# Kernel tuning notes

Hardware: AMD Instinct MI355X
Metric: run time of the kernel (lower is better)

The kernel has to match this reference:

```python
import jax, jax.numpy as jnp
import numpy as np

N_NODES = 100000
N_EDGES = 1600000
NUM_PROP = 5
CAT_PROP = 3
INPUT_DIM = 128
HIDDEN = 128
NUM_REL = 2


def setup_inputs() -> dict:
    key = jax.random.key(0)
    ks = jax.random.split(key, 20)
    s = 0.05
    inp = {
        "x": jax.random.normal(ks[0], (N_NODES, NUM_PROP + CAT_PROP), jnp.float32),
        "edge_index": jax.random.randint(ks[1], (2, N_EDGES), 0, N_NODES, jnp.int64 if jax.config.jax_enable_x64 else jnp.int32),
        "edge_type": jax.random.randint(ks[2], (N_EDGES,), 0, NUM_REL, jnp.int32),
        # numeric / categorical encoders -> input_dim/2 each
        "W_num": jax.random.normal(ks[3], (NUM_PROP, INPUT_DIM // 2), jnp.float32) * s,
        "b_num": jnp.zeros((INPUT_DIM // 2,), jnp.float32),
        "W_cat": jax.random.normal(ks[4], (CAT_PROP, INPUT_DIM // 2), jnp.float32) * s,
        "b_cat": jnp.zeros((INPUT_DIM // 2,), jnp.float32),
        # input projection + PReLU
        "W_in": jax.random.normal(ks[5], (INPUT_DIM, HIDDEN), jnp.float32) * s,
        "b_in": jnp.zeros((HIDDEN,), jnp.float32),
        "prelu_a": jnp.full((HIDDEN,), 0.25, jnp.float32),
        # RGCN layer 1
        "W_rel1": jax.random.normal(ks[6], (NUM_REL, HIDDEN, HIDDEN), jnp.float32) * s,
        "W_root1": jax.random.normal(ks[7], (HIDDEN, HIDDEN), jnp.float32) * s,
        "b_rgcn1": jnp.zeros((HIDDEN,), jnp.float32),
        # RGCN layer 2
        "W_rel2": jax.random.normal(ks[8], (NUM_REL, HIDDEN, HIDDEN), jnp.float32) * s,
        "W_root2": jax.random.normal(ks[9], (HIDDEN, HIDDEN), jnp.float32) * s,
        "b_rgcn2": jnp.zeros((HIDDEN,), jnp.float32),
        # classifier (single Linear)
        "W_cls": jax.random.normal(ks[10], (HIDDEN, HIDDEN), jnp.float32) * s,
        "b_cls": jnp.zeros((HIDDEN,), jnp.float32),
    }
    return inp


def _leaky_relu(x, slope=0.01):
    return jnp.where(x >= 0, x, slope * x)


def _prelu(x, a):
    return jnp.where(x >= 0, x, a * x)


def _rgcn_conv(x, edge_index, edge_type, W_rel, W_root, bias):
    # PyG RGCNConv: out[i] = x[i] @ W_root + bias + sum_r mean_{j in N_r(i)} x[j] @ W_r
    # Aggregate-then-transform (linearity) to avoid per-edge (E, d) @ W products.
    src, dst = edge_index[0], edge_index[1]
    n = x.shape[0]
    x_src = x[src]  # (E, d) gather
    out = x @ W_root + bias
    for r in range(W_rel.shape[0]):
        w = (edge_type == r).astype(x.dtype)  # (E,)
        agg = jax.ops.segment_sum(x_src * w[:, None], dst, num_segments=n)  # (N, d)
        deg = jax.ops.segment_sum(w, dst, num_segments=n)  # (N,)
        out = out + (agg / jnp.clip(deg, 1.0)[:, None]) @ W_rel[r]
    return out


def reference(x, edge_index, edge_type, W_num, b_num, W_cat, b_cat, W_in, b_in,
              prelu_a, W_rel1, W_root1, b_rgcn1, W_rel2, W_root2, b_rgcn2,
              W_cls, b_cls):
    num_prop = x[:, :NUM_PROP]
    cat_prop = x[:, NUM_PROP:NUM_PROP + CAT_PROP]
    n = _leaky_relu(num_prop @ W_num + b_num)
    c = _leaky_relu(cat_prop @ W_cat + b_cat)
    h = jnp.concatenate([n, c], axis=1)
    h = _prelu(h @ W_in + b_in, prelu_a)
    h = _rgcn_conv(h, edge_index, edge_type, W_rel1, W_root1, b_rgcn1)
    # dropout is identity in eval mode
    h = _rgcn_conv(h, edge_index, edge_type, W_rel2, W_root2, b_rgcn2)
    return h @ W_cls + b_cls
```

## Files before the change

### kernel.cpp

```cpp
#include <hip/hip_runtime.h>
#include <cstdint>


typedef short bf16x8 __attribute__((ext_vector_type(8)));
typedef float f32x4  __attribute__((ext_vector_type(4)));

__device__ __forceinline__ unsigned short f2bf(float f) {
    unsigned int u = __builtin_bit_cast(unsigned int, f);
    u += 0x7fff + ((u >> 16) & 1);
    return (unsigned short)(u >> 16);
}
__device__ __forceinline__ float bf2f(unsigned short h) {
    unsigned int u = ((unsigned int)h) << 16;
    return __builtin_bit_cast(float, u);
}
__device__ __forceinline__ float lo16f(unsigned int u) {
    return __builtin_bit_cast(float, u << 16);
}
__device__ __forceinline__ float hi16f(unsigned int u) {
    return __builtin_bit_cast(float, u & 0xffff0000u);
}

__device__ __forceinline__ void gload_lds16(const void* g, void* l) {
    __builtin_amdgcn_global_load_lds(
        (const __attribute__((address_space(1))) void*)g,
        (__attribute__((address_space(3))) void*)l, 16, 0, 0);
}

__global__ __launch_bounds__(256) void k_egemm(
    const float* __restrict__ x,
    const float* __restrict__ Wnum, const float* __restrict__ bnum,
    const float* __restrict__ Wcat, const float* __restrict__ bcat,
    const unsigned short* __restrict__ Bhi, const unsigned short* __restrict__ Blo,
    const float* __restrict__ bias, const float* __restrict__ prelu,
    unsigned short* __restrict__ C_hi, unsigned short* __restrict__ C_lo, int M)
{
    __shared__ unsigned short lds[2][32 * 512];
    const int t = threadIdx.x;
    const int w = t >> 6, lane = t & 63;
    const int laneL = lane & 15, laneH = lane >> 4;
    const int wi = w >> 1, wj = w & 1;
    const int m0 = blockIdx.x * 128;
    const int Mm1 = M - 1;

    f32x4 acc[4][4];
    #pragma unroll
    for (int a = 0; a < 4; ++a)
        #pragma unroll
        for (int b = 0; b < 4; ++b)
            acc[a][b] = (f32x4){0.f, 0.f, 0.f, 0.f};

    auto stage = [&](int s, unsigned short* buf) {
        int koff = s * 32;
        int k8 = koff + laneH * 8;
        #pragma unroll
        for (int c = 0; c < 2; ++c) {
            int j = w + c * 4;
            int rc = j * 16 + laneL;
            int row = (m0 + rc <= Mm1) ? (m0 + rc) : Mm1;
            const float4* xr = (const float4*)(x + (size_t)row * 8);
            float4 X0 = xr[0], X1 = xr[1];
            float a[8];
            if (k8 < 64) {
                const float4* bp = (const float4*)(bnum + k8);
                float4 b0 = bp[0], b1 = bp[1];
                a[0]=b0.x; a[1]=b0.y; a[2]=b0.z; a[3]=b0.w;
                a[4]=b1.x; a[5]=b1.y; a[6]=b1.z; a[7]=b1.w;
                float xs0 = X0.x, xs1 = X0.y, xs2 = X0.z, xs3 = X0.w, xs4 = X1.x;
                const float* wb = Wnum + k8;
                #pragma unroll
                for (int p = 0; p < 5; ++p) {
                    float xp = p==0?xs0 : p==1?xs1 : p==2?xs2 : p==3?xs3 : xs4;
                    const float4* wp = (const float4*)(wb + p * 64);
                    float4 w0 = wp[0], w1 = wp[1];
                    a[0]+=xp*w0.x; a[1]+=xp*w0.y; a[2]+=xp*w0.z; a[3]+=xp*w0.w;
                    a[4]+=xp*w1.x; a[5]+=xp*w1.y; a[6]+=xp*w1.z; a[7]+=xp*w1.w;
                }
            } else {
                int kk = k8 - 64;
                const float4* bp = (const float4*)(bcat + kk);
                float4 b0 = bp[0], b1 = bp[1];
                a[0]=b0.x; a[1]=b0.y; a[2]=b0.z; a[3]=b0.w;
                a[4]=b1.x; a[5]=b1.y; a[6]=b1.z; a[7]=b1.w;
                float xs0 = X1.y, xs1 = X1.z, xs2 = X1.w;
                const float* wb = Wcat + kk;
                #pragma unroll
                for (int p = 0; p < 3; ++p) {
                    float xp = p==0?xs0 : p==1?xs1 : xs2;
                    const float4* wp = (const float4*)(wb + p * 64);
                    float4 w0 = wp[0], w1 = wp[1];
                    a[0]+=xp*w0.x; a[1]+=xp*w0.y; a[2]+=xp*w0.z; a[3]+=xp*w0.w;
                    a[4]+=xp*w1.x; a[5]+=xp*w1.y; a[6]+=xp*w1.z; a[7]+=xp*w1.w;
                }
            }
            unsigned hw[4], lw[4];
            #pragma unroll
            for (int q = 0; q < 4; ++q) {
                float v0 = a[2*q]   >= 0.f ? a[2*q]   : 0.01f * a[2*q];
                float v1 = a[2*q+1] >= 0.f ? a[2*q+1] : 0.01f * a[2*q+1];
                unsigned short h0 = f2bf(v0), h1 = f2bf(v1);
                unsigned short l0 = f2bf(v0 - bf2f(h0)), l1 = f2bf(v1 - bf2f(h1));
                hw[q] = (unsigned)h0 | ((unsigned)h1 << 16);
                lw[q] = (unsigned)l0 | ((unsigned)l1 << 16);
            }
            uint4 ho, lo_;
            ho.x=hw[0]; ho.y=hw[1]; ho.z=hw[2]; ho.w=hw[3];
            lo_.x=lw[0]; lo_.y=lw[1]; lo_.z=lw[2]; lo_.w=lw[3];
            *(uint4*)&buf[(0 * 8 + j) * 512 + lane * 8] = ho;
            *(uint4*)&buf[(1 * 8 + j) * 512 + lane * 8] = lo_;
        }
        #pragma unroll
        for (int c = 4; c < 8; ++c) {
            int chunk = w + c * 4;
            int slot = chunk >> 3, j = chunk & 7;
            const unsigned short* plane = (slot == 2) ? Bhi : Blo;
            int rc = j * 16 + laneL;
            const unsigned short* gp = plane + (size_t)rc * 128 + koff + laneH * 8;
            gload_lds16(gp, &buf[(slot * 8 + j) * 512]);
        }
    };

    stage(0, lds[0]);
    for (int s = 0; s < 4; ++s) {
        unsigned short* cur = lds[s & 1];
        unsigned short* nxt = lds[(s & 1) ^ 1];
        __syncthreads();
        if (s + 1 < 4) stage(s + 1, nxt);
        const bf16x8* fr = (const bf16x8*)cur;
        bf16x8 ah[4], al[4], bh[4], bl[4];
        #pragma unroll
        for (int mi = 0; mi < 4; ++mi) {
            ah[mi] = fr[(0 + wi * 4 + mi) * 64 + lane];
            al[mi] = fr[(8 + wi * 4 + mi) * 64 + lane];
        }
        #pragma unroll
        for (int nj = 0; nj < 4; ++nj) {
            bh[nj] = fr[(16 + wj * 4 + nj) * 64 + lane];
            bl[nj] = fr[(24 + wj * 4 + nj) * 64 + lane];
        }
        #pragma unroll
        for (int mi = 0; mi < 4; ++mi)
            #pragma unroll
            for (int nj = 0; nj < 4; ++nj) {
                acc[mi][nj] = __builtin_amdgcn_mfma_f32_16x16x32_bf16(
                    ah[mi], bh[nj], acc[mi][nj], 0, 0, 0);
                acc[mi][nj] = __builtin_amdgcn_mfma_f32_16x16x32_bf16(
                    ah[mi], bl[nj], acc[mi][nj], 0, 0, 0);
                acc[mi][nj] = __builtin_amdgcn_mfma_f32_16x16x32_bf16(
                    al[mi], bh[nj], acc[mi][nj], 0, 0, 0);
            }
    }

    float bv[4], av[4];
    #pragma unroll
    for (int nj = 0; nj < 4; ++nj) {
        int col = wj * 64 + nj * 16 + laneL;
        bv[nj] = bias[col];
        av[nj] = prelu[col];
    }
    unsigned short* lph = &lds[0][0];
    unsigned short* lpl = &lds[1][0];
    __syncthreads();
    #pragma unroll
    for (int nj = 0; nj < 4; ++nj) {
        int col = wj * 64 + nj * 16 + laneL;
        #pragma unroll
        for (int mi = 0; mi < 4; ++mi)
            #pragma unroll
            for (int r = 0; r < 4; ++r) {
                int row = wi * 64 + mi * 16 + laneH * 4 + r;
                float v = acc[mi][nj][r] + bv[nj];
                v = v >= 0.f ? v : av[nj] * v;
                unsigned short h = f2bf(v);
                lph[row * 128 + col] = h;
                lpl[row * 128 + col] = f2bf(v - bf2f(h));
            }
    }
    __syncthreads();
    {
        const uint4* sh = (const uint4*)lph;
        const uint4* sl = (const uint4*)lpl;
        #pragma unroll
        for (int it = 0; it < 8; ++it) {
            int idx = it * 256 + t;
            int row = idx >> 4, c = idx & 15;
            int m = m0 + row;
            if (m < M) {
                ((uint4*)(C_hi + (size_t)m * 128))[c] = sh[idx];
                ((uint4*)(C_lo + (size_t)m * 128))[c] = sl[idx];
            }
        }
    }
}

struct WHArgs {
    const float* W[8];
    unsigned short* hi[8];
    unsigned short* lo[8];
    const int* ei;
    const int* et;
    int* cntmatT;
    int E;
    int N;
    int NBINS;
};
__global__ __launch_bounds__(256) void k_wsplit_hist(WHArgs a)
{
    __shared__ int hist[1024];
    const int t = threadIdx.x;
    const int b = blockIdx.x;
    if (b < 512) {
        int part = b >> 6;
        int idx = (b & 63) * 256 + t;
        int n = idx >> 7, k = idx & 127;
        float v = a.W[part][(size_t)k * 128 + n];
        unsigned short h = f2bf(v);
        a.hi[part][(size_t)n * 128 + k] = h;
        a.lo[part][(size_t)n * 128 + k] = f2bf(v - bf2f(h));
        return;
    }
    const int blk = b - 512;
    for (int i = t; i < a.NBINS; i += 256) hist[i] = 0;
    __syncthreads();
    #pragma unroll
    for (int j = 0; j < 16; ++j) {
        int e = blk * 4096 + j * 256 + t;
        if (e < a.E) atomicAdd(&hist[(a.et[e] * a.N + a.ei[a.E + e]) >> 8], 1);
    }
    __syncthreads();
    for (int i = t; i < a.NBINS; i += 256)
        a.cntmatT[(size_t)blk * a.NBINS + i] = hist[i];
}

__global__ __launch_bounds__(256) void k_transpose(
    const int* __restrict__ src, int* __restrict__ dst, int R, int C)
{
    __shared__ int tile[32][33];
    int ctiles = (C + 31) >> 5;
    int bx = blockIdx.x % ctiles;
    int by = blockIdx.x / ctiles;
    int tc = threadIdx.x & 31, tr = threadIdx.x >> 5;
    int c0 = bx * 32, r0 = by * 32;
    #pragma unroll
    for (int i = 0; i < 32; i += 8) {
        int r = r0 + tr + i, c = c0 + tc;
        if (r < R && c < C) tile[tr + i][tc] = src[(size_t)r * C + c];
    }
    __syncthreads();
    #pragma unroll
    for (int i = 0; i < 32; i += 8) {
        int r = r0 + tc;
        int c = c0 + tr + i;
        if (r < R && c < C) dst[(size_t)c * R + r] = tile[tc][tr + i];
    }
}

__global__ __launch_bounds__(256) void k_transpose_add(
    const int* __restrict__ src, int* __restrict__ dst,
    const int* __restrict__ bsum, int R, int C)
{
    __shared__ int tile[32][33];
    int ctiles = (C + 31) >> 5;
    int bx = blockIdx.x % ctiles;
    int by = blockIdx.x / ctiles;
    int tc = threadIdx.x & 31, tr = threadIdx.x >> 5;
    int c0 = bx * 32, r0 = by * 32;
    #pragma unroll
    for (int i = 0; i < 32; i += 8) {
        int r = r0 + tr + i, c = c0 + tc;
        if (r < R && c < C) {
            size_t idx = (size_t)r * C + c;
            tile[tr + i][tc] = src[idx] + bsum[idx >> 8];
        }
    }
    __syncthreads();
    #pragma unroll
    for (int i = 0; i < 32; i += 8) {
        int r = r0 + tc;
        int c = c0 + tr + i;
        if (r < R && c < C) dst[(size_t)c * R + r] = tile[tc][tr + i];
    }
}

__global__ __launch_bounds__(256) void k_scan1(
    const int* __restrict__ src, int* __restrict__ dst,
    int* __restrict__ bsum, int n)
{
    __shared__ int s[256];
    int t = threadIdx.x;
    int i = blockIdx.x * 256 + t;
    int v = (i < n) ? src[i] : 0;
    s[t] = v;
    __syncthreads();
    #pragma unroll
    for (int d = 1; d < 256; d <<= 1) {
        int add = (t >= d) ? s[t - d] : 0;
        __syncthreads();
        s[t] += add;
        __syncthreads();
    }
    if (i < n) dst[i] = s[t] - v;
    if (t == 255) bsum[blockIdx.x] = s[255];
}

__global__ __launch_bounds__(1024) void k_scan2(int* __restrict__ bsum, int nb)
{
    __shared__ int s[1024];
    int t = threadIdx.x;
    int carry = 0;
    for (int base = 0; base < nb; base += 1024) {
        int i = base + t;
        int v = (i < nb) ? bsum[i] : 0;
        s[t] = v;
        __syncthreads();
        #pragma unroll
        for (int d = 1; d < 1024; d <<= 1) {
            int add = (t >= d) ? s[t - d] : 0;
            __syncthreads();
            s[t] += add;
            __syncthreads();
        }
        if (i < nb) bsum[i] = carry + s[t] - v;
        carry += s[1023];
        __syncthreads();
    }
}

__global__ __launch_bounds__(256) void k_binscatter(
    const int* __restrict__ ei, const int* __restrict__ et,
    const int* __restrict__ cntscanT, int* __restrict__ ebuf,
    int E, int N, int NBINS)
{
    __shared__ int base[1024];
    const int t = threadIdx.x;
    const int blk = blockIdx.x;
    for (int i = t; i < NBINS; i += 256)
        base[i] = cntscanT[(size_t)blk * NBINS + i];
    __syncthreads();
    #pragma unroll
    for (int j = 0; j < 16; ++j) {
        int e = blk * 4096 + j * 256 + t;
        if (e < E) {
            unsigned src = (unsigned)ei[e];
            int seg = et[e] * N + ei[E + e];
            int pos = atomicAdd(&base[seg >> 8], 1);
            ebuf[pos] = (int)(((unsigned)(seg & 255) << 24) | src);
        }
    }
}

__global__ __launch_bounds__(256) void k_bincsr(
    const int* __restrict__ cntscan, const int* __restrict__ bsum,
    const int* __restrict__ ebuf,
    int* __restrict__ deg, int* __restrict__ off, int* __restrict__ esrc,
    int E, int nseg, int NBLK, int NBINS)
{
    __shared__ int cnt[256];
    __shared__ int pfx[256];
    __shared__ int cur[256];
    const int b = blockIdx.x;
    const int t = threadIdx.x;
    size_t i0 = (size_t)b * NBLK;
    const int est = cntscan[i0] + bsum[i0 >> 8];
    int een = E;
    if (b + 1 < NBINS) {
        size_t i1 = (size_t)(b + 1) * NBLK;
        een = cntscan[i1] + bsum[i1 >> 8];
    }
    cnt[t] = 0;
    __syncthreads();
    for (int e = est + t; e < een; e += 256)
        atomicAdd(&cnt[((unsigned)ebuf[e]) >> 24], 1);
    __syncthreads();
    int v = cnt[t];
    pfx[t] = v;
    __syncthreads();
    #pragma unroll
    for (int d = 1; d < 256; d <<= 1) {
        int add = (t >= d) ? pfx[t - d] : 0;
        __syncthreads();
        pfx[t] += add;
        __syncthreads();
    }
    int o = est + pfx[t] - v;
    int seg = b * 256 + t;
    if (seg < nseg) { deg[seg] = v; off[seg] = o; }
    cur[t] = o;
    __syncthreads();
    for (int e = est + t; e < een; e += 256) {
        unsigned u = (unsigned)ebuf[e];
        int p = atomicAdd(&cur[u >> 24], 1);
        esrc[p] = (int)(u & 0xffffffu);
    }
}

__global__ __launch_bounds__(256) void k_gather(
    const unsigned short* __restrict__ h_hi,
    const int* __restrict__ esrc,
    const int* __restrict__ off, const int* __restrict__ deg,
    unsigned short* __restrict__ a_hi, int nseg)
{
    int i = blockIdx.x * 8 + (threadIdx.x >> 5);
    if (i >= nseg) return;
    int l32 = threadIdx.x & 31;
    int q = l32 >> 4;
    int l16 = l32 & 15;
    int cnt = deg[i], st = off[i];
    const uint4* hp = (const uint4*)h_hi;
    float a0 = 0.f, a1 = 0.f, a2 = 0.f, a3 = 0.f;
    float a4 = 0.f, a5 = 0.f, a6 = 0.f, a7 = 0.f;
    int e = q;
    for (; e + 6 < cnt; e += 8) {
        int i0 = esrc[st + e + 0];
        int i1 = esrc[st + e + 2];
        int i2 = esrc[st + e + 4];
        int i3 = esrc[st + e + 6];
        uint4 u0 = hp[(size_t)i0 * 16 + l16];
        uint4 u1 = hp[(size_t)i1 * 16 + l16];
        uint4 u2 = hp[(size_t)i2 * 16 + l16];
        uint4 u3 = hp[(size_t)i3 * 16 + l16];
        a0 += lo16f(u0.x); a1 += hi16f(u0.x); a2 += lo16f(u0.y); a3 += hi16f(u0.y);
        a4 += lo16f(u0.z); a5 += hi16f(u0.z); a6 += lo16f(u0.w); a7 += hi16f(u0.w);
        a0 += lo16f(u1.x); a1 += hi16f(u1.x); a2 += lo16f(u1.y); a3 += hi16f(u1.y);
        a4 += lo16f(u1.z); a5 += hi16f(u1.z); a6 += lo16f(u1.w); a7 += hi16f(u1.w);
        a0 += lo16f(u2.x); a1 += hi16f(u2.x); a2 += lo16f(u2.y); a3 += hi16f(u2.y);
        a4 += lo16f(u2.z); a5 += hi16f(u2.z); a6 += lo16f(u2.w); a7 += hi16f(u2.w);
        a0 += lo16f(u3.x); a1 += hi16f(u3.x); a2 += lo16f(u3.y); a3 += hi16f(u3.y);
        a4 += lo16f(u3.z); a5 += hi16f(u3.z); a6 += lo16f(u3.w); a7 += hi16f(u3.w);
    }
    for (; e < cnt; e += 2) {
        uint4 u = hp[(size_t)esrc[st + e] * 16 + l16];
        a0 += lo16f(u.x); a1 += hi16f(u.x); a2 += lo16f(u.y); a3 += hi16f(u.y);
        a4 += lo16f(u.z); a5 += hi16f(u.z); a6 += lo16f(u.w); a7 += hi16f(u.w);
    }
    a0 += __shfl_xor(a0, 16, 64);
    a1 += __shfl_xor(a1, 16, 64);
    a2 += __shfl_xor(a2, 16, 64);
    a3 += __shfl_xor(a3, 16, 64);
    a4 += __shfl_xor(a4, 16, 64);
    a5 += __shfl_xor(a5, 16, 64);
    a6 += __shfl_xor(a6, 16, 64);
    a7 += __shfl_xor(a7, 16, 64);
    if (q == 0) {
        float inv = 1.0f / (float)(cnt > 1 ? cnt : 1);
        uint4 o;
        o.x = (unsigned int)f2bf(a0 * inv) | ((unsigned int)f2bf(a1 * inv) << 16);
        o.y = (unsigned int)f2bf(a2 * inv) | ((unsigned int)f2bf(a3 * inv) << 16);
        o.z = (unsigned int)f2bf(a4 * inv) | ((unsigned int)f2bf(a5 * inv) << 16);
        o.w = (unsigned int)f2bf(a6 * inv) | ((unsigned int)f2bf(a7 * inv) << 16);
        ((uint4*)a_hi)[(size_t)i * 16 + l16] = o;
    }
}

struct GArgs {
    const unsigned short* A_hi[3];
    const unsigned short* A_lo[3];
    const unsigned short* B_hi[3];
    const unsigned short* B_lo[3];
    int alo[3];
    int blo[3];
    const float* bias;
    const float* prelu;
    unsigned short* C_hi;
    unsigned short* C_lo;
    int M;
    int P;
    const unsigned short* clsBhi;
    const unsigned short* clsBlo;
    const float* clsBias;
    float* outF;
};

__global__ __launch_bounds__(256) void k_mgemm(GArgs g)
{
    __shared__ unsigned short lds[2][32 * 512];
    const int t = threadIdx.x;
    const int w = t >> 6, lane = t & 63;
    const int laneL = lane & 15, laneH = lane >> 4;
    const int wi = w >> 1, wj = w & 1;
    const int m0 = blockIdx.x * 128;
    const int Mm1 = g.M - 1;
    const int S = g.P * 4;

    f32x4 acc[4][4];
    #pragma unroll
    for (int a = 0; a < 4; ++a)
        #pragma unroll
        for (int b = 0; b < 4; ++b)
            acc[a][b] = (f32x4){0.f, 0.f, 0.f, 0.f};

    auto stage = [&](int s, unsigned short* buf) {
        int p = s >> 2, koff = (s & 3) * 32;
        const unsigned short* tp[4];
        tp[0] = g.A_hi[p];
        tp[1] = g.alo[p] ? g.A_lo[p] : nullptr;
        tp[2] = g.B_hi[p];
        tp[3] = g.blo[p] ? g.B_lo[p] : nullptr;
        #pragma unroll
        for (int c = 0; c < 8; ++c) {
            int chunk = w + c * 4;
            int slot = chunk >> 3, j = chunk & 7;
            const unsigned short* plane = tp[slot];
            if (!plane) continue;
            int rc = j * 16 + laneL;
            int row = (slot < 2) ? (m0 + rc <= Mm1 ? m0 + rc : Mm1) : rc;
            const unsigned short* gp = plane + (size_t)row * 128 + koff + laneH * 8;
            gload_lds16(gp, &buf[(slot * 8 + j) * 512]);
        }
    };

    stage(0, lds[0]);
    for (int s = 0; s < S; ++s) {
        unsigned short* cur = lds[s & 1];
        unsigned short* nxt = lds[(s & 1) ^ 1];
        __syncthreads();
        if (s + 1 < S) stage(s + 1, nxt);
        int p = s >> 2;
        const bool hasAlo = g.alo[p] != 0;
        const bool hasBlo = g.blo[p] != 0;
        const bf16x8* fr = (const bf16x8*)cur;
        bf16x8 ah[4], al[4], bh[4], bl[4];
        #pragma unroll
        for (int mi = 0; mi < 4; ++mi)
            ah[mi] = fr[(0 + wi * 4 + mi) * 64 + lane];
        if (hasAlo) {
            #pragma unroll
            for (int mi = 0; mi < 4; ++mi)
                al[mi] = fr[(8 + wi * 4 + mi) * 64 + lane];
        }
        #pragma unroll
        for (int nj = 0; nj < 4; ++nj)
            bh[nj] = fr[(16 + wj * 4 + nj) * 64 + lane];
        if (hasBlo) {
            #pragma unroll
            for (int nj = 0; nj < 4; ++nj)
                bl[nj] = fr[(24 + wj * 4 + nj) * 64 + lane];
        }
        #pragma unroll
        for (int mi = 0; mi < 4; ++mi)
            #pragma unroll
            for (int nj = 0; nj < 4; ++nj) {
                acc[mi][nj] = __builtin_amdgcn_mfma_f32_16x16x32_bf16(
                    ah[mi], bh[nj], acc[mi][nj], 0, 0, 0);
                if (hasBlo)
                    acc[mi][nj] = __builtin_amdgcn_mfma_f32_16x16x32_bf16(
                        ah[mi], bl[nj], acc[mi][nj], 0, 0, 0);
                if (hasAlo)
                    acc[mi][nj] = __builtin_amdgcn_mfma_f32_16x16x32_bf16(
                        al[mi], bh[nj], acc[mi][nj], 0, 0, 0);
            }
    }

    float bv[4];
    #pragma unroll
    for (int nj = 0; nj < 4; ++nj)
        bv[nj] = g.bias[wj * 64 + nj * 16 + laneL];

    if (g.clsBhi) {
        char* l0 = (char*)&lds[0][0];
        char* l1 = (char*)&lds[1][0];
        __syncthreads();
        #pragma unroll
        for (int nj = 0; nj < 4; ++nj) {
            int col = wj * 64 + nj * 16 + laneL;
            #pragma unroll
            for (int mi = 0; mi < 4; ++mi)
                #pragma unroll
                for (int r = 0; r < 4; ++r) {
                    int row = wi * 64 + mi * 16 + laneH * 4 + r;
                    float v = acc[mi][nj][r] + bv[nj];
                    unsigned short h = f2bf(v);
                    int offb = row * 256 + ((col * 2) ^ ((row & 7) << 4));
                    *(unsigned short*)(l0 + offb) = h;
                    *(unsigned short*)(l1 + offb) = f2bf(v - bf2f(h));
                }
        }
        __syncthreads();
        f32x4 acc2[4][4];
        #pragma unroll
        for (int a = 0; a < 4; ++a)
            #pragma unroll
            for (int b = 0; b < 4; ++b)
                acc2[a][b] = (f32x4){0.f, 0.f, 0.f, 0.f};
        #pragma unroll
        for (int ks = 0; ks < 4; ++ks) {
            bf16x8 ah2[4], al2[4], bh2[4], bl2[4];
            #pragma unroll
            for (int mi = 0; mi < 4; ++mi) {
                int rc = wi * 64 + mi * 16 + laneL;
                int aoff = rc * 256 + ((ks * 64 + laneH * 16) ^ ((rc & 7) << 4));
                ah2[mi] = *(const bf16x8*)(l0 + aoff);
                al2[mi] = *(const bf16x8*)(l1 + aoff);
            }
            #pragma unroll
            for (int nj = 0; nj < 4; ++nj) {
                int rc = wj * 64 + nj * 16 + laneL;
                size_t boff = (size_t)rc * 128 + ks * 32 + laneH * 8;
                bh2[nj] = *(const bf16x8*)(g.clsBhi + boff);
                bl2[nj] = *(const bf16x8*)(g.clsBlo + boff);
            }
            #pragma unroll
            for (int mi = 0; mi < 4; ++mi)
                #pragma unroll
                for (int nj = 0; nj < 4; ++nj) {
                    acc2[mi][nj] = __builtin_amdgcn_mfma_f32_16x16x32_bf16(
                        ah2[mi], bh2[nj], acc2[mi][nj], 0, 0, 0);
                    acc2[mi][nj] = __builtin_amdgcn_mfma_f32_16x16x32_bf16(
                        ah2[mi], bl2[nj], acc2[mi][nj], 0, 0, 0);
                    acc2[mi][nj] = __builtin_amdgcn_mfma_f32_16x16x32_bf16(
                        al2[mi], bh2[nj], acc2[mi][nj], 0, 0, 0);
                }
        }
        float cb[4];
        #pragma unroll
        for (int nj = 0; nj < 4; ++nj)
            cb[nj] = g.clsBias[wj * 64 + nj * 16 + laneL];
        float* lf = (float*)&lds[0][0];
        __syncthreads();
        #pragma unroll
        for (int nj = 0; nj < 4; ++nj) {
            int col = wj * 64 + nj * 16 + laneL;
            #pragma unroll
            for (int mi = 0; mi < 4; ++mi)
                #pragma unroll
                for (int r = 0; r < 4; ++r) {
                    int row = wi * 64 + mi * 16 + laneH * 4 + r;
                    lf[row * 128 + col] = acc2[mi][nj][r] + cb[nj];
                }
        }
        __syncthreads();
        const uint4* lsrc = (const uint4*)lf;
        #pragma unroll
        for (int it = 0; it < 16; ++it) {
            int idx = it * 256 + t;
            int row = idx >> 5, c = idx & 31;
            int m = m0 + row;
            if (m < g.M)
                ((uint4*)(g.outF + (size_t)m * 128))[c] = lsrc[idx];
        }
        return;
    }

    const bool hasPrelu = (g.prelu != nullptr);
    float av[4];
    #pragma unroll
    for (int nj = 0; nj < 4; ++nj)
        av[nj] = hasPrelu ? g.prelu[wj * 64 + nj * 16 + laneL] : 0.f;

    unsigned short* lph = &lds[0][0];
    unsigned short* lpl = &lds[1][0];
    __syncthreads();
    #pragma unroll
    for (int nj = 0; nj < 4; ++nj) {
        int col = wj * 64 + nj * 16 + laneL;
        #pragma unroll
        for (int mi = 0; mi < 4; ++mi)
            #pragma unroll
            for (int r = 0; r < 4; ++r) {
                int row = wi * 64 + mi * 16 + laneH * 4 + r;
                float v = acc[mi][nj][r] + bv[nj];
                if (hasPrelu) v = v >= 0.f ? v : av[nj] * v;
                unsigned short h = f2bf(v);
                lph[row * 128 + col] = h;
                lpl[row * 128 + col] = f2bf(v - bf2f(h));
            }
    }
    __syncthreads();
    {
        const uint4* sh = (const uint4*)lph;
        const uint4* sl = (const uint4*)lpl;
        #pragma unroll
        for (int it = 0; it < 8; ++it) {
            int idx = it * 256 + t;
            int row = idx >> 4, c = idx & 15;
            int m = m0 + row;
            if (m < g.M) {
                ((uint4*)(g.C_hi + (size_t)m * 128))[c] = sh[idx];
                ((uint4*)(g.C_lo + (size_t)m * 128))[c] = sl[idx];
            }
        }
    }
}

extern "C" void kernel_launch(void* const* d_in, const int* in_sizes, int n_in,
                              void* d_out, int out_size, void* d_ws, size_t ws_size,
                              hipStream_t stream) {
    const float* x      = (const float*)d_in[0];
    const int*   ei     = (const int*)d_in[1];
    const int*   et     = (const int*)d_in[2];
    const float* Wnum   = (const float*)d_in[3];
    const float* bnum   = (const float*)d_in[4];
    const float* Wcat   = (const float*)d_in[5];
    const float* bcat   = (const float*)d_in[6];
    const float* Win    = (const float*)d_in[7];
    const float* bin    = (const float*)d_in[8];
    const float* pa     = (const float*)d_in[9];
    const float* Wrel1  = (const float*)d_in[10];
    const float* Wroot1 = (const float*)d_in[11];
    const float* brg1   = (const float*)d_in[12];
    const float* Wrel2  = (const float*)d_in[13];
    const float* Wroot2 = (const float*)d_in[14];
    const float* brg2   = (const float*)d_in[15];
    const float* Wcls   = (const float*)d_in[16];
    const float* bcls   = (const float*)d_in[17];
    float* out = (float*)d_out;

    const int N = in_sizes[0] / 8;
    const int E = in_sizes[1] / 2;
    const int nseg = 2 * N;
    const size_t NH = (size_t)N * 128;

    const int NBLK  = (E + 4095) / 4096;
    const int NBINS = (nseg + 255) / 256;
    const long long L = (long long)NBINS * NBLK;

    char* w = (char*)d_ws;
    unsigned short* h1_hi = (unsigned short*)w;  w += NH * 2;
    unsigned short* h1_lo = (unsigned short*)w;  w += NH * 2;
    unsigned short* agg_hi = (unsigned short*)w; w += 2 * NH * 2;
    int* deg      = (int*)w;  w += (size_t)nseg * 4;
    int* off      = (int*)w;  w += (size_t)nseg * 4;
    int* cntmatT  = (int*)w;  w += (size_t)L * 4;
    int* cntmat   = (int*)w;  w += (size_t)L * 4;
    int* cntscan  = (int*)w;  w += (size_t)L * 4;
    int* cntscanT = (int*)w;  w += (size_t)L * 4;
    int* esrc     = (int*)w;  w += (size_t)E * 4;
    int* bsum     = (int*)w;  w += 4096 * 4;
    unsigned short* wplanes = (unsigned short*)w;  w += 8 * 2 * 16384 * 2;

    int* ebuf = (int*)d_out;
    unsigned short* h0_hi = (unsigned short*)d_out;
    unsigned short* h0_lo = h0_hi + NH;

    unsigned short* whi[8];
    unsigned short* wlo[8];
    for (int i = 0; i < 8; ++i) {
        whi[i] = wplanes + (size_t)i * 2 * 16384;
        wlo[i] = whi[i] + 16384;
    }

    const int gm = (N + 127) / 128;
    const int gg = (nseg + 7) / 8;

    {
        WHArgs a;
        a.W[0] = Win;   a.W[1] = Wroot1; a.W[2] = Wrel1; a.W[3] = Wrel1 + 16384;
        a.W[4] = Wroot2; a.W[5] = Wrel2; a.W[6] = Wrel2 + 16384; a.W[7] = Wcls;
        for (int i = 0; i < 8; ++i) { a.hi[i] = whi[i]; a.lo[i] = wlo[i]; }
        a.ei = ei; a.et = et; a.cntmatT = cntmatT;
        a.E = E; a.N = N; a.NBINS = NBINS;
        k_wsplit_hist<<<512 + NBLK, 256, 0, stream>>>(a);
    }

    k_transpose<<<((NBLK + 31) / 32) * ((NBINS + 31) / 32), 256, 0, stream>>>(
        cntmatT, cntmat, NBLK, NBINS);

    const int nb1 = (int)((L + 255) / 256);
    k_scan1<<<nb1, 256, 0, stream>>>(cntmat, cntscan, bsum, (int)L);
    k_scan2<<<1, 1024, 0, stream>>>(bsum, nb1);
    k_transpose_add<<<((NBINS + 31) / 32) * ((NBLK + 31) / 32), 256, 0, stream>>>(
        cntscan, cntscanT, bsum, NBINS, NBLK);

    k_binscatter<<<NBLK, 256, 0, stream>>>(ei, et, cntscanT, ebuf, E, N, NBINS);
    k_bincsr<<<NBINS, 256, 0, stream>>>(cntscan, bsum, ebuf, deg, off, esrc,
                                        E, nseg, NBLK, NBINS);

    k_egemm<<<gm, 256, 0, stream>>>(x, Wnum, bnum, Wcat, bcat,
                                    whi[0], wlo[0], bin, pa,
                                    h0_hi, h0_lo, N);

    k_gather<<<gg, 256, 0, stream>>>(h0_hi, esrc, off, deg, agg_hi, nseg);
    {
        GArgs g = {};
        g.A_hi[0] = h0_hi;       g.A_lo[0] = h0_lo;  g.alo[0] = 1; g.blo[0] = 1;
        g.A_hi[1] = agg_hi;      g.alo[1] = 0;       g.blo[1] = 0;
        g.A_hi[2] = agg_hi + NH; g.alo[2] = 0;       g.blo[2] = 0;
        g.B_hi[0] = whi[1]; g.B_lo[0] = wlo[1];
        g.B_hi[1] = whi[2]; g.B_lo[1] = wlo[2];
        g.B_hi[2] = whi[3]; g.B_lo[2] = wlo[3];
        g.bias = brg1; g.prelu = nullptr;
        g.C_hi = h1_hi; g.C_lo = h1_lo;
        g.M = N; g.P = 3;
        g.clsBhi = nullptr;
        k_mgemm<<<gm, 256, 0, stream>>>(g);
    }
    k_gather<<<gg, 256, 0, stream>>>(h1_hi, esrc, off, deg, agg_hi, nseg);
    {
        GArgs g = {};
        g.A_hi[0] = h1_hi;       g.A_lo[0] = h1_lo;  g.alo[0] = 1; g.blo[0] = 1;
        g.A_hi[1] = agg_hi;      g.alo[1] = 0;       g.blo[1] = 0;
        g.A_hi[2] = agg_hi + NH; g.alo[2] = 0;       g.blo[2] = 0;
        g.B_hi[0] = whi[4]; g.B_lo[0] = wlo[4];
        g.B_hi[1] = whi[5]; g.B_lo[1] = wlo[5];
        g.B_hi[2] = whi[6]; g.B_lo[2] = wlo[6];
        g.bias = brg2; g.prelu = nullptr;
        g.C_hi = nullptr; g.C_lo = nullptr;
        g.M = N; g.P = 3;
        g.clsBhi = whi[7]; g.clsBlo = wlo[7];
        g.clsBias = bcls; g.outF = out;
        k_mgemm<<<gm, 256, 0, stream>>>(g);
    }
}
```

Baseline: 436.3 us.

## Halve GEMM LDS footprint by reading weights from global and splitting epilogues

The GEMM kernels no longer stage the B (weight) tiles in shared memory. Each wave now loads its B fragments straight from global memory, which is expected to be L2-resident, so the LDS buffers shrink by half. The epilogues write the hi and lo bf16 planes in two passes through a single buffer. The classifier path becomes its own kernel that keeps the lo plane packed in registers and runs the second GEMM in two phases, which removes the runtime branching. The aim is more resident blocks per CU from the smaller LDS footprint, at the cost of extra global loads, more barriers, and more register pressure in the classifier kernel.

```diff
diff --git a/kernel.cpp b/kernel.cpp
--- a/kernel.cpp
+++ b/kernel.cpp
@@ -35,7 +35,7 @@
     const float* __restrict__ bias, const float* __restrict__ prelu,
     unsigned short* __restrict__ C_hi, unsigned short* __restrict__ C_lo, int M)
 {
-    __shared__ unsigned short lds[2][32 * 512];
+    __shared__ unsigned short lds[2][16 * 512];
     const int t = threadIdx.x;
     const int w = t >> 6, lane = t & 63;
     const int laneL = lane & 15, laneH = lane >> 4;
@@ -107,16 +107,7 @@
             ho.x=hw[0]; ho.y=hw[1]; ho.z=hw[2]; ho.w=hw[3];
             lo_.x=lw[0]; lo_.y=lw[1]; lo_.z=lw[2]; lo_.w=lw[3];
             *(uint4*)&buf[(0 * 8 + j) * 512 + lane * 8] = ho;
-            *(uint4*)&buf[(1 * 8 + j) * 512 + lane * 8] = lo_;
-        }
-        #pragma unroll
-        for (int c = 4; c < 8; ++c) {
-            int chunk = w + c * 4;
-            int slot = chunk >> 3, j = chunk & 7;
-            const unsigned short* plane = (slot == 2) ? Bhi : Blo;
-            int rc = j * 16 + laneL;
-            const unsigned short* gp = plane + (size_t)rc * 128 + koff + laneH * 8;
-            gload_lds16(gp, &buf[(slot * 8 + j) * 512]);
+            *(uint4*)&buf[(8 + j) * 512 + lane * 8] = lo_;
         }
     };
 
@@ -126,6 +117,7 @@
         unsigned short* nxt = lds[(s & 1) ^ 1];
         __syncthreads();
         if (s + 1 < 4) stage(s + 1, nxt);
+        int koff = s * 32;
         const bf16x8* fr = (const bf16x8*)cur;
         bf16x8 ah[4], al[4], bh[4], bl[4];
         #pragma unroll
@@ -135,8 +127,9 @@
         }
         #pragma unroll
         for (int nj = 0; nj < 4; ++nj) {
-            bh[nj] = fr[(16 + wj * 4 + nj) * 64 + lane];
-            bl[nj] = fr[(24 + wj * 4 + nj) * 64 + lane];
+            size_t boff = (size_t)(wj * 64 + nj * 16 + laneL) * 128 + koff + laneH * 8;
+            bh[nj] = *(const bf16x8*)(Bhi + boff);
+            bl[nj] = *(const bf16x8*)(Blo + boff);
         }
         #pragma unroll
         for (int mi = 0; mi < 4; ++mi)
@@ -158,37 +151,34 @@
         bv[nj] = bias[col];
         av[nj] = prelu[col];
     }
-    unsigned short* lph = &lds[0][0];
-    unsigned short* lpl = &lds[1][0];
-    __syncthreads();
-    #pragma unroll
-    for (int nj = 0; nj < 4; ++nj) {
-        int col = wj * 64 + nj * 16 + laneL;
-        #pragma unroll
-        for (int mi = 0; mi < 4; ++mi)
-            #pragma unroll
-            for (int r = 0; r < 4; ++r) {
-                int row = wi * 64 + mi * 16 + laneH * 4 + r;
-                float v = acc[mi][nj][r] + bv[nj];
-                v = v >= 0.f ? v : av[nj] * v;
-                unsigned short h = f2bf(v);
-                lph[row * 128 + col] = h;
-                lpl[row * 128 + col] = f2bf(v - bf2f(h));
-            }
-    }
-    __syncthreads();
-    {
-        const uint4* sh = (const uint4*)lph;
-        const uint4* sl = (const uint4*)lpl;
+    unsigned short* lp = &lds[0][0];
+    #pragma unroll
+    for (int pass = 0; pass < 2; ++pass) {
+        __syncthreads();
+        #pragma unroll
+        for (int nj = 0; nj < 4; ++nj) {
+            int col = wj * 64 + nj * 16 + laneL;
+            #pragma unroll
+            for (int mi = 0; mi < 4; ++mi)
+                #pragma unroll
+                for (int r = 0; r < 4; ++r) {
+                    int row = wi * 64 + mi * 16 + laneH * 4 + r;
+                    float v = acc[mi][nj][r] + bv[nj];
+                    v = v >= 0.f ? v : av[nj] * v;
+                    unsigned short h = f2bf(v);
+                    lp[row * 128 + col] = pass == 0 ? h : f2bf(v - bf2f(h));
+                }
+        }
+        __syncthreads();
+        unsigned short* dst = pass == 0 ? C_hi : C_lo;
+        const uint4* lsrc = (const uint4*)lp;
         #pragma unroll
         for (int it = 0; it < 8; ++it) {
             int idx = it * 256 + t;
             int row = idx >> 4, c = idx & 15;
             int m = m0 + row;
-            if (m < M) {
-                ((uint4*)(C_hi + (size_t)m * 128))[c] = sh[idx];
-                ((uint4*)(C_lo + (size_t)m * 128))[c] = sl[idx];
-            }
+            if (m < M)
+                ((uint4*)(dst + (size_t)m * 128))[c] = lsrc[idx];
         }
     }
 }
@@ -460,7 +450,6 @@
     int alo[3];
     int blo[3];
     const float* bias;
-    const float* prelu;
     unsigned short* C_hi;
     unsigned short* C_lo;
     int M;
@@ -473,7 +462,7 @@
 
 __global__ __launch_bounds__(256) void k_mgemm(GArgs g)
 {
-    __shared__ unsigned short lds[2][32 * 512];
+    __shared__ unsigned short lds[2][16 * 512];
     const int t = threadIdx.x;
     const int w = t >> 6, lane = t & 63;
     const int laneL = lane & 15, laneH = lane >> 4;
@@ -491,21 +480,19 @@
 
     auto stage = [&](int s, unsigned short* buf) {
         int p = s >> 2, koff = (s & 3) * 32;
-        const unsigned short* tp[4];
-        tp[0] = g.A_hi[p];
-        tp[1] = g.alo[p] ? g.A_lo[p] : nullptr;
-        tp[2] = g.B_hi[p];
-        tp[3] = g.blo[p] ? g.B_lo[p] : nullptr;
-        #pragma unroll
-        for (int c = 0; c < 8; ++c) {
+        const unsigned short* tpA[2];
+        tpA[0] = g.A_hi[p];
+        tpA[1] = g.alo[p] ? g.A_lo[p] : nullptr;
+        #pragma unroll
+        for (int c = 0; c < 4; ++c) {
             int chunk = w + c * 4;
             int slot = chunk >> 3, j = chunk & 7;
-            const unsigned short* plane = tp[slot];
+            const unsigned short* plane = tpA[slot];
             if (!plane) continue;
             int rc = j * 16 + laneL;
-            int row = (slot < 2) ? (m0 + rc <= Mm1 ? m0 + rc : Mm1) : rc;
-            const unsigned short* gp = plane + (size_t)row * 128 + koff + laneH * 8;
-            gload_lds16(gp, &buf[(slot * 8 + j) * 512]);
+            int row = (m0 + rc <= Mm1) ? (m0 + rc) : Mm1;
+            gload_lds16(plane + (size_t)row * 128 + koff + laneH * 8,
+                        &buf[(slot * 8 + j) * 512]);
         }
     };
 
@@ -515,7 +502,7 @@
         unsigned short* nxt = lds[(s & 1) ^ 1];
         __syncthreads();
         if (s + 1 < S) stage(s + 1, nxt);
-        int p = s >> 2;
+        int p = s >> 2, koff = (s & 3) * 32;
         const bool hasAlo = g.alo[p] != 0;
         const bool hasBlo = g.blo[p] != 0;
         const bf16x8* fr = (const bf16x8*)cur;
@@ -528,13 +515,13 @@
             for (int mi = 0; mi < 4; ++mi)
                 al[mi] = fr[(8 + wi * 4 + mi) * 64 + lane];
         }
-        #pragma unroll
-        for (int nj = 0; nj < 4; ++nj)
-            bh[nj] = fr[(16 + wj * 4 + nj) * 64 + lane];
-        if (hasBlo) {
-            #pragma unroll
-            for (int nj = 0; nj < 4; ++nj)
-                bl[nj] = fr[(24 + wj * 4 + nj) * 64 + lane];
+        const unsigned short* Bh = g.B_hi[p];
+        const unsigned short* Bl = g.B_lo[p];
+        #pragma unroll
+        for (int nj = 0; nj < 4; ++nj) {
+            size_t boff = (size_t)(wj * 64 + nj * 16 + laneL) * 128 + koff + laneH * 8;
+            bh[nj] = *(const bf16x8*)(Bh + boff);
+            if (hasBlo) bl[nj] = *(const bf16x8*)(Bl + boff);
         }
         #pragma unroll
         for (int mi = 0; mi < 4; ++mi)
@@ -555,10 +542,9 @@
     #pragma unroll
     for (int nj = 0; nj < 4; ++nj)
         bv[nj] = g.bias[wj * 64 + nj * 16 + laneL];
-
-    if (g.clsBhi) {
-        char* l0 = (char*)&lds[0][0];
-        char* l1 = (char*)&lds[1][0];
+    unsigned short* lp = &lds[0][0];
+    #pragma unroll
+    for (int pass = 0; pass < 2; ++pass) {
         __syncthreads();
         #pragma unroll
         for (int nj = 0; nj < 4; ++nj) {
@@ -570,114 +556,231 @@
                     int row = wi * 64 + mi * 16 + laneH * 4 + r;
                     float v = acc[mi][nj][r] + bv[nj];
                     unsigned short h = f2bf(v);
-                    int offb = row * 256 + ((col * 2) ^ ((row & 7) << 4));
-                    *(unsigned short*)(l0 + offb) = h;
-                    *(unsigned short*)(l1 + offb) = f2bf(v - bf2f(h));
+                    lp[row * 128 + col] = pass == 0 ? h : f2bf(v - bf2f(h));
                 }
         }
         __syncthreads();
-        f32x4 acc2[4][4];
-        #pragma unroll
-        for (int a = 0; a < 4; ++a)
-            #pragma unroll
-            for (int b = 0; b < 4; ++b)
-                acc2[a][b] = (f32x4){0.f, 0.f, 0.f, 0.f};
-        #pragma unroll
-        for (int ks = 0; ks < 4; ++ks) {
-            bf16x8 ah2[4], al2[4], bh2[4], bl2[4];
-            #pragma unroll
-            for (int mi = 0; mi < 4; ++mi) {
-                int rc = wi * 64 + mi * 16 + laneL;
-                int aoff = rc * 256 + ((ks * 64 + laneH * 16) ^ ((rc & 7) << 4));
-                ah2[mi] = *(const bf16x8*)(l0 + aoff);
-                al2[mi] = *(const bf16x8*)(l1 + aoff);
-            }
-            #pragma unroll
-            for (int nj = 0; nj < 4; ++nj) {
-                int rc = wj * 64 + nj * 16 + laneL;
-                size_t boff = (size_t)rc * 128 + ks * 32 + laneH * 8;
-                bh2[nj] = *(const bf16x8*)(g.clsBhi + boff);
-                bl2[nj] = *(const bf16x8*)(g.clsBlo + boff);
-            }
-            #pragma unroll
-            for (int mi = 0; mi < 4; ++mi)
-                #pragma unroll
-                for (int nj = 0; nj < 4; ++nj) {
-                    acc2[mi][nj] = __builtin_amdgcn_mfma_f32_16x16x32_bf16(
-                        ah2[mi], bh2[nj], acc2[mi][nj], 0, 0, 0);
-                    acc2[mi][nj] = __builtin_amdgcn_mfma_f32_16x16x32_bf16(
-                        ah2[mi], bl2[nj], acc2[mi][nj], 0, 0, 0);
-                    acc2[mi][nj] = __builtin_amdgcn_mfma_f32_16x16x32_bf16(
-                        al2[mi], bh2[nj], acc2[mi][nj], 0, 0, 0);
-                }
-        }
-        float cb[4];
-        #pragma unroll
-        for (int nj = 0; nj < 4; ++nj)
-            cb[nj] = g.clsBias[wj * 64 + nj * 16 + laneL];
-        float* lf = (float*)&lds[0][0];
-        __syncthreads();
-        #pragma unroll
-        for (int nj = 0; nj < 4; ++nj) {
-            int col = wj * 64 + nj * 16 + laneL;
-            #pragma unroll
-            for (int mi = 0; mi < 4; ++mi)
-                #pragma unroll
-                for (int r = 0; r < 4; ++r) {
-                    int row = wi * 64 + mi * 16 + laneH * 4 + r;
-                    lf[row * 128 + col] = acc2[mi][nj][r] + cb[nj];
-                }
-        }
-        __syncthreads();
-        const uint4* lsrc = (const uint4*)lf;
-        #pragma unroll
-        for (int it = 0; it < 16; ++it) {
-            int idx = it * 256 + t;
-            int row = idx >> 5, c = idx & 31;
-            int m = m0 + row;
-            if (m < g.M)
-                ((uint4*)(g.outF + (size_t)m * 128))[c] = lsrc[idx];
-        }
-        return;
-    }
-
-    const bool hasPrelu = (g.prelu != nullptr);
-    float av[4];
-    #pragma unroll
-    for (int nj = 0; nj < 4; ++nj)
-        av[nj] = hasPrelu ? g.prelu[wj * 64 + nj * 16 + laneL] : 0.f;
-
-    unsigned short* lph = &lds[0][0];
-    unsigned short* lpl = &lds[1][0];
-    __syncthreads();
-    #pragma unroll
-    for (int nj = 0; nj < 4; ++nj) {
-        int col = wj * 64 + nj * 16 + laneL;
-        #pragma unroll
-        for (int mi = 0; mi < 4; ++mi)
-            #pragma unroll
-            for (int r = 0; r < 4; ++r) {
-                int row = wi * 64 + mi * 16 + laneH * 4 + r;
-                float v = acc[mi][nj][r] + bv[nj];
-                if (hasPrelu) v = v >= 0.f ? v : av[nj] * v;
-                unsigned short h = f2bf(v);
-                lph[row * 128 + col] = h;
-                lpl[row * 128 + col] = f2bf(v - bf2f(h));
-            }
-    }
-    __syncthreads();
-    {
-        const uint4* sh = (const uint4*)lph;
-        const uint4* sl = (const uint4*)lpl;
+        unsigned short* dst = pass == 0 ? g.C_hi : g.C_lo;
+        const uint4* lsrc = (const uint4*)lp;
         #pragma unroll
         for (int it = 0; it < 8; ++it) {
             int idx = it * 256 + t;
             int row = idx >> 4, c = idx & 15;
             int m = m0 + row;
-            if (m < g.M) {
-                ((uint4*)(g.C_hi + (size_t)m * 128))[c] = sh[idx];
-                ((uint4*)(g.C_lo + (size_t)m * 128))[c] = sl[idx];
+            if (m < g.M)
+                ((uint4*)(dst + (size_t)m * 128))[c] = lsrc[idx];
+        }
+    }
+}
+
+__global__ __launch_bounds__(256) void k_mgemm_cls(GArgs g)
+{
+    __shared__ unsigned short lds[2][16 * 512];
+    const int t = threadIdx.x;
+    const int w = t >> 6, lane = t & 63;
+    const int laneL = lane & 15, laneH = lane >> 4;
+    const int wi = w >> 1, wj = w & 1;
+    const int m0 = blockIdx.x * 128;
+    const int Mm1 = g.M - 1;
+    const int S = g.P * 4;
+
+    f32x4 acc[4][4];
+    #pragma unroll
+    for (int a = 0; a < 4; ++a)
+        #pragma unroll
+        for (int b = 0; b < 4; ++b)
+            acc[a][b] = (f32x4){0.f, 0.f, 0.f, 0.f};
+
+    auto stage = [&](int s, unsigned short* buf) {
+        int p = s >> 2, koff = (s & 3) * 32;
+        const unsigned short* tpA[2];
+        tpA[0] = g.A_hi[p];
+        tpA[1] = g.alo[p] ? g.A_lo[p] : nullptr;
+        #pragma unroll
+        for (int c = 0; c < 4; ++c) {
+            int chunk = w + c * 4;
+            int slot = chunk >> 3, j = chunk & 7;
+            const unsigned short* plane = tpA[slot];
+            if (!plane) continue;
+            int rc = j * 16 + laneL;
+            int row = (m0 + rc <= Mm1) ? (m0 + rc) : Mm1;
+            gload_lds16(plane + (size_t)row * 128 + koff + laneH * 8,
+                        &buf[(slot * 8 + j) * 512]);
+        }
+    };
+
+    stage(0, lds[0]);
+    for (int s = 0; s < S; ++s) {
+        unsigned short* cur = lds[s & 1];
+        unsigned short* nxt = lds[(s & 1) ^ 1];
+        __syncthreads();
+        if (s + 1 < S) stage(s + 1, nxt);
+        int p = s >> 2, koff = (s & 3) * 32;
+        const bool hasAlo = g.alo[p] != 0;
+        const bool hasBlo = g.blo[p] != 0;
+        const bf16x8* fr = (const bf16x8*)cur;
+        bf16x8 ah[4], al[4], bh[4], bl[4];
+        #pragma unroll
+        for (int mi = 0; mi < 4; ++mi)
+            ah[mi] = fr[(0 + wi * 4 + mi) * 64 + lane];
+        if (hasAlo) {
+            #pragma unroll
+            for (int mi = 0; mi < 4; ++mi)
+                al[mi] = fr[(8 + wi * 4 + mi) * 64 + lane];
+        }
+        const unsigned short* Bh = g.B_hi[p];
+        const unsigned short* Bl = g.B_lo[p];
+        #pragma unroll
+        for (int nj = 0; nj < 4; ++nj) {
+            size_t boff = (size_t)(wj * 64 + nj * 16 + laneL) * 128 + koff + laneH * 8;
+            bh[nj] = *(const bf16x8*)(Bh + boff);
+            if (hasBlo) bl[nj] = *(const bf16x8*)(Bl + boff);
+        }
+        #pragma unroll
+        for (int mi = 0; mi < 4; ++mi)
+            #pragma unroll
+            for (int nj = 0; nj < 4; ++nj) {
+                acc[mi][nj] = __builtin_amdgcn_mfma_f32_16x16x32_bf16(
+                    ah[mi], bh[nj], acc[mi][nj], 0, 0, 0);
+                if (hasBlo)
+                    acc[mi][nj] = __builtin_amdgcn_mfma_f32_16x16x32_bf16(
+                        ah[mi], bl[nj], acc[mi][nj], 0, 0, 0);
+                if (hasAlo)
+                    acc[mi][nj] = __builtin_amdgcn_mfma_f32_16x16x32_bf16(
+                        al[mi], bh[nj], acc[mi][nj], 0, 0, 0);
             }
+    }
+
+    float bv[4];
+    #pragma unroll
+    for (int nj = 0; nj < 4; ++nj)
+        bv[nj] = g.bias[wj * 64 + nj * 16 + laneL];
+
+    char* pl = (char*)&lds[0][0];
+    unsigned lopack[4][4][2];
+
+    __syncthreads();
+    #pragma unroll
+    for (int nj = 0; nj < 4; ++nj) {
+        int col = wj * 64 + nj * 16 + laneL;
+        #pragma unroll
+        for (int mi = 0; mi < 4; ++mi)
+            #pragma unroll
+            for (int r = 0; r < 4; ++r) {
+                int row = wi * 64 + mi * 16 + laneH * 4 + r;
+                float v = acc[mi][nj][r] + bv[nj];
+                unsigned short h = f2bf(v);
+                unsigned short l = f2bf(v - bf2f(h));
+                int offb = row * 256 + ((col * 2) ^ ((row & 7) << 4));
+                *(unsigned short*)(pl + offb) = h;
+                if (r & 1) lopack[nj][mi][r >> 1] |= (unsigned)l << 16;
+                else       lopack[nj][mi][r >> 1] = l;
+            }
+    }
+    __syncthreads();
+
+    f32x4 acc2[4][4];
+    #pragma unroll
+    for (int a = 0; a < 4; ++a)
+        #pragma unroll
+        for (int b = 0; b < 4; ++b)
+            acc2[a][b] = (f32x4){0.f, 0.f, 0.f, 0.f};
+
+    #pragma unroll
+    for (int ks = 0; ks < 4; ++ks) {
+        bf16x8 ah2[4], bh2[4], bl2[4];
+        #pragma unroll
+        for (int mi = 0; mi < 4; ++mi) {
+            int rc = wi * 64 + mi * 16 + laneL;
+            int aoff = rc * 256 + ((ks * 64 + laneH * 16) ^ ((rc & 7) << 4));
+            ah2[mi] = *(const bf16x8*)(pl + aoff);
+        }
+        #pragma unroll
+        for (int nj = 0; nj < 4; ++nj) {
+            size_t boff = (size_t)(wj * 64 + nj * 16 + laneL) * 128 + ks * 32 + laneH * 8;
+            bh2[nj] = *(const bf16x8*)(g.clsBhi + boff);
+            bl2[nj] = *(const bf16x8*)(g.clsBlo + boff);
+        }
+        #pragma unroll
+        for (int mi = 0; mi < 4; ++mi)
+            #pragma unroll
+            for (int nj = 0; nj < 4; ++nj) {
+                acc2[mi][nj] = __builtin_amdgcn_mfma_f32_16x16x32_bf16(
+                    ah2[mi], bh2[nj], acc2[mi][nj], 0, 0, 0);
+                acc2[mi][nj] = __builtin_amdgcn_mfma_f32_16x16x32_bf16(
+                    ah2[mi], bl2[nj], acc2[mi][nj], 0, 0, 0);
+            }
+    }
+    __syncthreads();
+
+    #pragma unroll
+    for (int nj = 0; nj < 4; ++nj) {
+        int col = wj * 64 + nj * 16 + laneL;
+        #pragma unroll
+        for (int mi = 0; mi < 4; ++mi)
+            #pragma unroll
+            for (int r = 0; r < 4; ++r) {
+                int row = wi * 64 + mi * 16 + laneH * 4 + r;
+                unsigned short l = (r & 1) ? (unsigned short)(lopack[nj][mi][r >> 1] >> 16)
+                                           : (unsigned short)(lopack[nj][mi][r >> 1] & 0xffff);
+                int offb = row * 256 + ((col * 2) ^ ((row & 7) << 4));
+                *(unsigned short*)(pl + offb) = l;
+            }
+    }
+    __syncthreads();
+
+    #pragma unroll
+    for (int ks = 0; ks < 4; ++ks) {
+        bf16x8 al2[4], bh2[4];
+        #pragma unroll
+        for (int mi = 0; mi < 4; ++mi) {
+            int rc = wi * 64 + mi * 16 + laneL;
+            int aoff = rc * 256 + ((ks * 64 + laneH * 16) ^ ((rc & 7) << 4));
+            al2[mi] = *(const bf16x8*)(pl + aoff);
+        }
+        #pragma unroll
+        for (int nj = 0; nj < 4; ++nj) {
+            size_t boff = (size_t)(wj * 64 + nj * 16 + laneL) * 128 + ks * 32 + laneH * 8;
+            bh2[nj] = *(const bf16x8*)(g.clsBhi + boff);
+        }
+        #pragma unroll
+        for (int mi = 0; mi < 4; ++mi)
+            #pragma unroll
+            for (int nj = 0; nj < 4; ++nj)
+                acc2[mi][nj] = __builtin_amdgcn_mfma_f32_16x16x32_bf16(
+                    al2[mi], bh2[nj], acc2[mi][nj], 0, 0, 0);
+    }
+
+    float cb[4];
+    #pragma unroll
+    for (int nj = 0; nj < 4; ++nj)
+        cb[nj] = g.clsBias[wj * 64 + nj * 16 + laneL];
+    float* lf = (float*)&lds[0][0];
+    #pragma unroll
+    for (int half = 0; half < 2; ++half) {
+        __syncthreads();
+        if (wi == half) {
+            #pragma unroll
+            for (int nj = 0; nj < 4; ++nj) {
+                int col = wj * 64 + nj * 16 + laneL;
+                #pragma unroll
+                for (int mi = 0; mi < 4; ++mi)
+                    #pragma unroll
+                    for (int r = 0; r < 4; ++r) {
+                        int lrow = mi * 16 + laneH * 4 + r;
+                        lf[lrow * 128 + col] = acc2[mi][nj][r] + cb[nj];
+                    }
+            }
+        }
+        __syncthreads();
+        const uint4* lsrc = (const uint4*)lf;
+        #pragma unroll
+        for (int it = 0; it < 8; ++it) {
+            int idx = it * 256 + t;
+            int row = idx >> 5, c = idx & 31;
+            int m = m0 + half * 64 + row;
+            if (m < g.M)
+                ((uint4*)(g.outF + (size_t)m * 128))[c] = lsrc[idx];
         }
     }
 }
@@ -778,10 +881,9 @@
         g.B_hi[0] = whi[1]; g.B_lo[0] = wlo[1];
         g.B_hi[1] = whi[2]; g.B_lo[1] = wlo[2];
         g.B_hi[2] = whi[3]; g.B_lo[2] = wlo[3];
-        g.bias = brg1; g.prelu = nullptr;
+        g.bias = brg1;
         g.C_hi = h1_hi; g.C_lo = h1_lo;
         g.M = N; g.P = 3;
-        g.clsBhi = nullptr;
         k_mgemm<<<gm, 256, 0, stream>>>(g);
     }
     k_gather<<<gg, 256, 0, stream>>>(h1_hi, esrc, off, deg, agg_hi, nseg);
@@ -793,11 +895,10 @@
         g.B_hi[0] = whi[4]; g.B_lo[0] = wlo[4];
         g.B_hi[1] = whi[5]; g.B_lo[1] = wlo[5];
         g.B_hi[2] = whi[6]; g.B_lo[2] = wlo[6];
-        g.bias = brg2; g.prelu = nullptr;
-        g.C_hi = nullptr; g.C_lo = nullptr;
+        g.bias = brg2;
         g.M = N; g.P = 3;
         g.clsBhi = whi[7]; g.clsBlo = wlo[7];
         g.clsBias = bcls; g.outF = out;
-        k_mgemm<<<gm, 256, 0, stream>>>(g);
-    }
-}
+        k_mgemm_cls<<<gm, 256, 0, stream>>>(g);
+    }
+}
```

Result: slower. 518.5 us (+18.8%).
